# Kernel tuning notes

Measured on AMD Instinct MI355X. Metric: run time of the kernel, lower is better.

The kernel has to match this reference:

```python
import jax, jax.numpy as jnp
import numpy as np
from jax import lax

# Problem constants (match input_specs / init_kwargs)
B, N, F_IN = 16, 4096, 64          # clouds, points per cloud, feature dim
RATIO, R, K = 0.25, 0.1, 64        # fps ratio, ball radius, max neighbors
S = int(N * RATIO)                 # sampled centers per cloud (1024)
H1, H2, OUT = 64, 64, 128          # MLP [F_IN+3 -> 64 -> 64 -> 128]


def _fps(pos):
    """Farthest point sampling on one cloud. pos: [N,3] -> idx [S] (start at 0)."""
    def step(carry, _):
        mind, last = carry
        d = jnp.sum((pos - pos[last]) ** 2, axis=-1)
        mind = jnp.minimum(mind, d)
        nxt = jnp.argmax(mind)
        return (mind, nxt), nxt
    init = (jnp.full((pos.shape[0],), jnp.inf, pos.dtype), jnp.array(0))
    _, rest = lax.scan(step, init, None, length=S - 1)
    return jnp.concatenate([jnp.zeros((1,), rest.dtype), rest])


def _mlp(h, W1, b1, W2, b2, W3, b3):
    h = jax.nn.relu(h @ W1 + b1)
    h = jax.nn.relu(h @ W2 + b2)
    return jax.nn.relu(h @ W3 + b3)


def setup_inputs() -> dict:
    key = jax.random.key(0)
    ks = jax.random.split(key, 8)
    x = jax.random.normal(ks[0], (B * N, F_IN), jnp.float32)
    pos = jax.random.uniform(ks[1], (B * N, 3), jnp.float32)  # unit cube
    batch = jnp.arange(B * N, dtype=jnp.int64) // N           # cloud ids, equal-size clouds
    d_in = F_IN + 3
    W1 = jax.random.normal(ks[2], (d_in, H1), jnp.float32) / np.sqrt(d_in)
    b1 = jnp.zeros((H1,), jnp.float32)
    W2 = jax.random.normal(ks[3], (H1, H2), jnp.float32) / np.sqrt(H1)
    b2 = jnp.zeros((H2,), jnp.float32)
    W3 = jax.random.normal(ks[4], (H2, OUT), jnp.float32) / np.sqrt(H2)
    b3 = jnp.zeros((OUT,), jnp.float32)
    return {"x": x, "pos": pos, "batch": batch,
            "W1": W1, "b1": b1, "W2": W2, "b2": b2, "W3": W3, "b3": b3}


def reference(x, pos, batch, W1, b1, W2, b2, W3, b3):
    xb = x.reshape(B, N, F_IN)
    pb = pos.reshape(B, N, 3)
    # --- fps(pos, batch, ratio) : per-cloud farthest point sampling ---
    idx = jax.vmap(_fps)(pb)                                   # [B,S]
    pos_s = jnp.take_along_axis(pb, idx[:, :, None], axis=1)   # [B,S,3]
    # --- radius(pos, pos[idx], r, max_num_neighbors=K) : ball query ---
    d2 = jnp.sum((pos_s[:, :, None, :] - pb[:, None, :, :]) ** 2, axis=-1)  # [B,S,N]
    neg = jnp.where(d2 <= R * R, -d2, -jnp.inf)
    vals, nbr = lax.top_k(neg, K)                              # [B,S,K] nearest-in-ball
    valid = jnp.isfinite(vals)                                 # center is its own neighbor -> >=1 valid
    # --- PointNetConv: msg = nn(concat(x_j, pos_j - pos_i)), max aggregation ---
    x_j = jax.vmap(lambda a, i: a[i])(xb, nbr)                 # [B,S,K,F_IN]
    p_j = jax.vmap(lambda a, i: a[i])(pb, nbr)                 # [B,S,K,3]
    msg = jnp.concatenate([x_j, p_j - pos_s[:, :, None, :]], axis=-1)
    m = _mlp(msg, W1, b1, W2, b2, W3, b3)                      # [B,S,K,OUT]
    m = jnp.where(valid[..., None], m, -jnp.inf)
    out = jnp.max(m, axis=2)                                   # [B,S,OUT]
    batch_s = jnp.take_along_axis(batch.reshape(B, N), idx, axis=1).reshape(-1)
    return out.reshape(B * S, OUT), pos_s.reshape(B * S, 3), batch_s
```

## Files before the change

### kernel.cpp

```cpp
#include <hip/hip_runtime.h>
#include <hip/hip_bf16.h>
#include <math.h>


#define NB 16
#define NP 4096
#define FIN 64
#define NS 1024
#define KN 64
#define CAP 128
#define NCONS 240
#define NCHUNK 4096

typedef __attribute__((ext_vector_type(8))) short bf16x8;
typedef __attribute__((ext_vector_type(4))) float f32x4;

__device__ __forceinline__ float dist2e(float ax, float ay, float az,
                                        float bx, float by, float bz) {
    float dx = __fsub_rn(ax, bx);
    float dy = __fsub_rn(ay, by);
    float dz = __fsub_rn(az, bz);
    return __fadd_rn(__fadd_rn(__fmul_rn(dx, dx), __fmul_rn(dy, dy)),
                     __fmul_rn(dz, dz));
}

__device__ __forceinline__ short f2bf(float f) {
    unsigned u = __float_as_uint(f);
    unsigned r = (u + 0x7FFFu + ((u >> 16) & 1u)) >> 16;
    return (short)r;
}

#define DPP_KEY_MAX(k, CTRL)                                                   \
    do {                                                                       \
        int _lo = (int)(unsigned)((k) & 0xFFFFFFFFull);                        \
        int _hi = (int)(unsigned)((k) >> 32);                                  \
        int _plo = __builtin_amdgcn_update_dpp(_lo, _lo, CTRL, 0xF, 0xF, false);\
        int _phi = __builtin_amdgcn_update_dpp(_hi, _hi, CTRL, 0xF, 0xF, false);\
        unsigned long long _nk =                                               \
            ((unsigned long long)(unsigned)_phi << 32) | (unsigned)_plo;       \
        if (_nk > (k)) (k) = _nk;                                              \
    } while (0)

#define WAVE_KEY_MAX(k)                                                        \
    do {                                                                       \
        DPP_KEY_MAX(k, 0x121);                                                 \
        DPP_KEY_MAX(k, 0x122);                                                 \
        DPP_KEY_MAX(k, 0x124);                                                 \
        DPP_KEY_MAX(k, 0x128);                                                 \
        {                                                                      \
            int _lo = (int)(unsigned)((k) & 0xFFFFFFFFull);                    \
            int _hi = (int)(unsigned)((k) >> 32);                              \
            int _plo = __builtin_amdgcn_ds_swizzle(_lo, 0x401F);               \
            int _phi = __builtin_amdgcn_ds_swizzle(_hi, 0x401F);               \
            unsigned long long _nk =                                           \
                ((unsigned long long)(unsigned)_phi << 32) | (unsigned)_plo;   \
            if (_nk > (k)) (k) = _nk;                                          \
        }                                                                      \
        {                                                                      \
            unsigned long long _nk = __shfl_xor((k), 32, 64);                  \
            if (_nk > (k)) (k) = _nk;                                          \
        }                                                                      \
    } while (0)

#define SMEM_BYTES 65792

__global__ __launch_bounds__(256, 1) void fused_kernel(
        const float* __restrict__ pos, const float* __restrict__ x,
        const float* __restrict__ W1, const float* __restrict__ b1,
        const float* __restrict__ W2, const float* __restrict__ b2,
        const float* __restrict__ W3, const float* __restrict__ b3,
        float* __restrict__ out_feat, float* __restrict__ out_pos,
        float* __restrict__ out_batch, float* __restrict__ histg,
        int* __restrict__ progress) {
    __shared__ __align__(16) char smem[SMEM_BYTES];
    const int tid = threadIdx.x;
    const int lane = tid & 63;
    const int wv = tid >> 6;

    if (blockIdx.x < NB) {
        const int b = blockIdx.x;
        float* px = (float*)smem;
        float* py = (float*)(smem + 16384);
        float* pz = (float*)(smem + 32768);
        float4* hist = (float4*)(smem + 49152);
        float (*bc)[4][8] = (float(*)[4][8])(smem + 65536);
        const float* p = pos + (size_t)b * NP * 3;
        float lx[16], ly[16], lz[16], md[16];
#pragma unroll
        for (int i = 0; i < 16; ++i) {
            int j = tid + (i << 8);
            float xx = p[j * 3 + 0];
            float yy = p[j * 3 + 1];
            float zz = p[j * 3 + 2];
            px[j] = xx; py[j] = yy; pz[j] = zz;
            lx[i] = xx; ly[i] = yy; lz[i] = zz;
            md[i] = INFINITY;
        }
        __syncthreads();
        const float c0x = px[0], c0y = py[0], c0z = pz[0];
        float cx = c0x, cy = c0y, cz = c0z;
        if (tid == 0) hist[0] = make_float4(0.f, c0x, c0y, c0z);
        for (int s = 1; s < NS; ++s) {
            float bv = -1.0f;
            int bi = 0;
#pragma unroll
            for (int i = 0; i < 16; ++i) {
                float d = dist2e(lx[i], ly[i], lz[i], cx, cy, cz);
                float m = md[i];
                m = d < m ? d : m;
                md[i] = m;
                bool take = (m > bv);
                bv = take ? m : bv;
                bi = take ? (tid + (i << 8)) : bi;
            }
            unsigned long long key =
                ((unsigned long long)__float_as_uint(bv) << 32) |
                (unsigned)(~(unsigned)bi);
            WAVE_KEY_MAX(key);
            const int buf = s & 1;
            if (lane == 0) {
                int wi = (int)(~(unsigned)(key & 0xFFFFFFFFull));
                bc[buf][wv][0] =
                    __uint_as_float((unsigned)(key & 0xFFFFFFFFull));
                bc[buf][wv][1] = __uint_as_float((unsigned)(key >> 32));
                bc[buf][wv][2] = px[wi];
                bc[buf][wv][3] = py[wi];
                bc[buf][wv][4] = pz[wi];
            }
            __syncthreads();
            if ((s & 63) == 0) {
                const int base = s - 64;
                if (tid < 192) {
                    int cc = tid / 3, comp = tid % 3;
                    float4 h = hist[base + cc];
                    float v = comp == 0 ? h.y : (comp == 1 ? h.z : h.w);
                    __hip_atomic_store(
                        (unsigned*)&histg[((size_t)(b * NS + base + cc)) * 3 + comp],
                        __float_as_uint(v), __ATOMIC_RELAXED,
                        __HIP_MEMORY_SCOPE_AGENT);
                }
                __syncthreads();
                if (tid == 0)
                    __hip_atomic_store(&progress[b << 5], s, __ATOMIC_RELEASE,
                                       __HIP_MEMORY_SCOPE_AGENT);
            }
            unsigned long long bk;
            float bx, by, bz;
            {
                float4 e = *(const float4*)&bc[buf][0][0];
                bk = ((unsigned long long)__float_as_uint(e.y) << 32) |
                     __float_as_uint(e.x);
                bx = e.z; by = e.w; bz = bc[buf][0][4];
            }
#pragma unroll
            for (int w = 1; w < 4; ++w) {
                float4 e = *(const float4*)&bc[buf][w][0];
                unsigned long long k2 =
                    ((unsigned long long)__float_as_uint(e.y) << 32) |
                    __float_as_uint(e.x);
                float z2 = bc[buf][w][4];
                bool take = (k2 > bk);
                bk = take ? k2 : bk;
                bx = take ? e.z : bx;
                by = take ? e.w : by;
                bz = take ? z2 : bz;
            }
            const int cur = (int)(~(unsigned)(bk & 0xFFFFFFFFull));
            cx = bx; cy = by; cz = bz;
            if (tid == 0)
                hist[s] = make_float4(__int_as_float(cur), bx, by, bz);
        }
        __syncthreads();
        if (tid < 192) {
            int cc = tid / 3, comp = tid % 3;
            float4 h = hist[960 + cc];
            float v = comp == 0 ? h.y : (comp == 1 ? h.z : h.w);
            __hip_atomic_store(
                (unsigned*)&histg[((size_t)(b * NS + 960 + cc)) * 3 + comp],
                __float_as_uint(v), __ATOMIC_RELAXED, __HIP_MEMORY_SCOPE_AGENT);
        }
        __syncthreads();
        if (tid == 0)
            __hip_atomic_store(&progress[b << 5], NS, __ATOMIC_RELEASE,
                               __HIP_MEMORY_SCOPE_AGENT);
        for (int s = tid; s < NS; s += 256) {
            float4 e = hist[s];
            out_pos[(size_t)(b * NS + s) * 3 + 0] = e.y;
            out_pos[(size_t)(b * NS + s) * 3 + 1] = e.z;
            out_pos[(size_t)(b * NS + s) * 3 + 2] = e.w;
            out_batch[b * NS + s] = (float)b;
        }
        return;
    }

    const int w = blockIdx.x - NB;
    short* h1s = (short*)smem;
    short* h2s = (short*)(smem + 8192);
    float* cd2 = (float*)(smem + 16384);
    int*   cix = (int*)(smem + 18432);
    float* dpxA = (float*)(smem + 20480);
    float* dpyA = (float*)(smem + 21504);
    float* dpzA = (float*)(smem + 22528);
    int*   jA   = (int*)(smem + 23552);
    float* omax = (float*)(smem + 24576);
    int*   keepW = (int*)(smem + 26624);
    const int lg = lane >> 4;
    const int lr = lane & 15;
    bf16x8 w1f[3][4], w2f[2][4], w3f[2][8];
#pragma unroll
    for (int kt = 0; kt < 3; ++kt)
#pragma unroll
        for (int ct = 0; ct < 4; ++ct) {
            bf16x8 f;
#pragma unroll
            for (int i = 0; i < 8; ++i) {
                int k = 32 * kt + 8 * lg + i;
                float v = (k < 67) ? W1[k * 64 + 16 * ct + lr] : 0.f;
                f[i] = f2bf(v);
            }
            w1f[kt][ct] = f;
        }
#pragma unroll
    for (int kt = 0; kt < 2; ++kt)
#pragma unroll
        for (int ct = 0; ct < 4; ++ct) {
            bf16x8 f;
#pragma unroll
            for (int i = 0; i < 8; ++i) {
                int k = 32 * kt + 8 * lg + i;
                f[i] = f2bf(W2[k * 64 + 16 * ct + lr]);
            }
            w2f[kt][ct] = f;
        }
#pragma unroll
    for (int kt = 0; kt < 2; ++kt)
#pragma unroll
        for (int ct = 0; ct < 8; ++ct) {
            bf16x8 f;
#pragma unroll
            for (int i = 0; i < 8; ++i) {
                int k = 32 * kt + 8 * lg + i;
                f[i] = f2bf(W3[k * 128 + 16 * ct + lr]);
            }
            w3f[kt][ct] = f;
        }
    float b1v[4], b2v[4], b3v[8];
#pragma unroll
    for (int ct = 0; ct < 4; ++ct) {
        b1v[ct] = b1[16 * ct + lr];
        b2v[ct] = b2[16 * ct + lr];
    }
#pragma unroll
    for (int ct = 0; ct < 8; ++ct) b3v[ct] = b3[16 * ct + lr];

    for (int c = w; c < NCHUNK; c += NCONS) {
        const int s = c >> 2;
        const int bq = (c & 3) << 2;
        const int bw = bq + wv;
        while (__hip_atomic_load(&progress[bw << 5], __ATOMIC_ACQUIRE,
                                 __HIP_MEMORY_SCOPE_AGENT) <= s) {
            __builtin_amdgcn_s_sleep(16);
        }
        const size_t ho = ((size_t)(bw * NS + s)) * 3;
        const float ccx = __uint_as_float(__hip_atomic_load(
            (const unsigned*)&histg[ho + 0], __ATOMIC_RELAXED,
            __HIP_MEMORY_SCOPE_AGENT));
        const float ccy = __uint_as_float(__hip_atomic_load(
            (const unsigned*)&histg[ho + 1], __ATOMIC_RELAXED,
            __HIP_MEMORY_SCOPE_AGENT));
        const float ccz = __uint_as_float(__hip_atomic_load(
            (const unsigned*)&histg[ho + 2], __ATOMIC_RELAXED,
            __HIP_MEMORY_SCOPE_AGENT));
        int cnt = 0;
        const float* pcloud = pos + (size_t)bw * NP * 3;
        for (int it = 0; it < 64; ++it) {
            const int j = it * 64 + lane;
            const float* pp = pcloud + (size_t)j * 3;
            float d2 = dist2e(ccx, ccy, ccz, pp[0], pp[1], pp[2]);
            bool in = (d2 <= 0.01f);
            unsigned long long m = __ballot(in);
            if (in) {
                int slot = cnt + __popcll(m & ((1ull << lane) - 1ull));
                if (slot < CAP) {
                    cd2[wv * CAP + slot] = d2;
                    cix[wv * CAP + slot] = j;
                }
            }
            cnt += __popcll(m);
        }
        if (cnt > CAP) cnt = CAP;
        const int keep = cnt <= KN ? cnt : KN;
        if (lane == 0) keepW[wv] = keep;
        jA[wv * 64 + lane] = 0;
        if (cnt <= KN) {
            if (lane < keep) jA[wv * 64 + lane] = cix[wv * CAP + lane];
        } else {
            for (int e = lane; e < cnt; e += 64) {
                float d = cd2[wv * CAP + e];
                int id = cix[wv * CAP + e];
                int rank = 0;
                for (int q = 0; q < cnt; ++q) {
                    float dq = cd2[wv * CAP + q];
                    int iq = cix[wv * CAP + q];
                    rank += (dq < d || (dq == d && iq < id)) ? 1 : 0;
                }
                if (rank < KN) jA[wv * 64 + rank] = id;
            }
        }
        {
            int j = jA[wv * 64 + lane];
            const float* pp = pcloud + (size_t)j * 3;
            bool valid = lane < keep;
            dpxA[wv * 64 + lane] = valid ? (pp[0] - ccx) : 0.f;
            dpyA[wv * 64 + lane] = valid ? (pp[1] - ccy) : 0.f;
            dpzA[wv * 64 + lane] = valid ? (pp[2] - ccz) : 0.f;
        }
        __syncthreads();
        for (int cc = 0; cc < 4; ++cc) {
            const int C = keepW[cc];
            const int cen = (bq + cc) * NS + s;
            const int arow = 16 * wv + lr;
            bf16x8 a0, a1, a2;
            {
                const int jrow = (bq + cc) * NP + jA[cc * 64 + arow];
                const float* xr = x + (size_t)jrow * FIN + 8 * lg;
                float4 v0 = *(const float4*)(xr + 0);
                float4 v1 = *(const float4*)(xr + 4);
                float4 v2 = *(const float4*)(xr + 32);
                float4 v3 = *(const float4*)(xr + 36);
                a0[0] = f2bf(v0.x); a0[1] = f2bf(v0.y); a0[2] = f2bf(v0.z); a0[3] = f2bf(v0.w);
                a0[4] = f2bf(v1.x); a0[5] = f2bf(v1.y); a0[6] = f2bf(v1.z); a0[7] = f2bf(v1.w);
                a1[0] = f2bf(v2.x); a1[1] = f2bf(v2.y); a1[2] = f2bf(v2.z); a1[3] = f2bf(v2.w);
                a1[4] = f2bf(v3.x); a1[5] = f2bf(v3.y); a1[6] = f2bf(v3.z); a1[7] = f2bf(v3.w);
                float d0 = (lg == 0) ? dpxA[cc * 64 + arow] : 0.f;
                float d1 = (lg == 0) ? dpyA[cc * 64 + arow] : 0.f;
                float d2v = (lg == 0) ? dpzA[cc * 64 + arow] : 0.f;
                a2[0] = f2bf(d0); a2[1] = f2bf(d1); a2[2] = f2bf(d2v);
                a2[3] = 0; a2[4] = 0; a2[5] = 0; a2[6] = 0; a2[7] = 0;
            }
            {
                f32x4 acc[4];
#pragma unroll
                for (int ct = 0; ct < 4; ++ct) {
                    acc[ct] = (f32x4){b1v[ct], b1v[ct], b1v[ct], b1v[ct]};
                    acc[ct] = __builtin_amdgcn_mfma_f32_16x16x32_bf16(a0, w1f[0][ct], acc[ct], 0, 0, 0);
                    acc[ct] = __builtin_amdgcn_mfma_f32_16x16x32_bf16(a1, w1f[1][ct], acc[ct], 0, 0, 0);
                    acc[ct] = __builtin_amdgcn_mfma_f32_16x16x32_bf16(a2, w1f[2][ct], acc[ct], 0, 0, 0);
                }
#pragma unroll
                for (int ct = 0; ct < 4; ++ct)
#pragma unroll
                    for (int r = 0; r < 4; ++r) {
                        int rw = 16 * wv + 4 * lg + r;
                        int idx = rw * 64 + 16 * ct + lr;
                        h1s[idx ^ ((rw & 7) << 3)] = f2bf(fmaxf(acc[ct][r], 0.f));
                    }
            }
            bf16x8 ha0 = *(bf16x8*)&h1s[(arow * 64 + 0  + 8 * lg) ^ ((arow & 7) << 3)];
            bf16x8 ha1 = *(bf16x8*)&h1s[(arow * 64 + 32 + 8 * lg) ^ ((arow & 7) << 3)];
            {
                f32x4 acc[4];
#pragma unroll
                for (int ct = 0; ct < 4; ++ct) {
                    acc[ct] = (f32x4){b2v[ct], b2v[ct], b2v[ct], b2v[ct]};
                    acc[ct] = __builtin_amdgcn_mfma_f32_16x16x32_bf16(ha0, w2f[0][ct], acc[ct], 0, 0, 0);
                    acc[ct] = __builtin_amdgcn_mfma_f32_16x16x32_bf16(ha1, w2f[1][ct], acc[ct], 0, 0, 0);
                }
#pragma unroll
                for (int ct = 0; ct < 4; ++ct)
#pragma unroll
                    for (int r = 0; r < 4; ++r) {
                        int rw = 16 * wv + 4 * lg + r;
                        int idx = rw * 64 + 16 * ct + lr;
                        h2s[idx ^ ((rw & 7) << 3)] = f2bf(fmaxf(acc[ct][r], 0.f));
                    }
            }
            bf16x8 hb0 = *(bf16x8*)&h2s[(arow * 64 + 0  + 8 * lg) ^ ((arow & 7) << 3)];
            bf16x8 hb1 = *(bf16x8*)&h2s[(arow * 64 + 32 + 8 * lg) ^ ((arow & 7) << 3)];
            {
                f32x4 acc3[8];
#pragma unroll
                for (int ct = 0; ct < 8; ++ct) {
                    acc3[ct] = (f32x4){b3v[ct], b3v[ct], b3v[ct], b3v[ct]};
                    acc3[ct] = __builtin_amdgcn_mfma_f32_16x16x32_bf16(hb0, w3f[0][ct], acc3[ct], 0, 0, 0);
                    acc3[ct] = __builtin_amdgcn_mfma_f32_16x16x32_bf16(hb1, w3f[1][ct], acc3[ct], 0, 0, 0);
                }
#pragma unroll
                for (int ct = 0; ct < 8; ++ct) {
                    float m = -INFINITY;
#pragma unroll
                    for (int r = 0; r < 4; ++r) {
                        int rg = 16 * wv + 4 * lg + r;
                        float v = fmaxf(acc3[ct][r], 0.f);
                        m = (rg < C && v > m) ? v : m;
                    }
                    m = fmaxf(m, __shfl_xor(m, 16, 64));
                    m = fmaxf(m, __shfl_xor(m, 32, 64));
                    if (lg == 0) omax[wv * 128 + 16 * ct + lr] = m;
                }
            }
            __syncthreads();
            if (tid < 128) {
                float m = fmaxf(fmaxf(omax[0 * 128 + tid], omax[1 * 128 + tid]),
                                fmaxf(omax[2 * 128 + tid], omax[3 * 128 + tid]));
                out_feat[(size_t)cen * 128 + tid] = m;
            }
            __syncthreads();
        }
    }
}

extern "C" void kernel_launch(void* const* d_in, const int* in_sizes, int n_in,
                              void* d_out, int out_size, void* d_ws, size_t ws_size,
                              hipStream_t stream) {
    const float* x   = (const float*)d_in[0];
    const float* pos = (const float*)d_in[1];
    const float* W1  = (const float*)d_in[3];
    const float* b1  = (const float*)d_in[4];
    const float* W2  = (const float*)d_in[5];
    const float* b2  = (const float*)d_in[6];
    const float* W3  = (const float*)d_in[7];
    const float* b3  = (const float*)d_in[8];
    float* out = (float*)d_out;
    char* ws = (char*)d_ws;
    int*   progress = (int*)ws;
    float* histg    = (float*)(ws + 4096);
    float* out_feat  = out;
    float* out_pos   = out + (size_t)16384 * 128;
    float* out_batch = out + (size_t)16384 * 131;
    hipMemsetAsync(ws, 0, 4096, stream);
    fused_kernel<<<256, 256, 0, stream>>>(pos, x, W1, b1, W2, b2, W3, b3,
                                          out_feat, out_pos, out_batch,
                                          histg, progress);
}
```

Baseline: 1.009 ms.

## Run FPS on a single wave with packed math, offload publishing to a second wave

```diff
diff --git a/kernel.cpp b/kernel.cpp
--- a/kernel.cpp
+++ b/kernel.cpp
@@ -14,6 +14,7 @@
 
 typedef __attribute__((ext_vector_type(8))) short bf16x8;
 typedef __attribute__((ext_vector_type(4))) float f32x4;
+typedef __attribute__((ext_vector_type(2))) float f32x2;
 
 __device__ __forceinline__ float dist2e(float ax, float ay, float az,
                                         float bx, float by, float bz) {
@@ -62,7 +63,7 @@
         }                                                                      \
     } while (0)
 
-#define SMEM_BYTES 65792
+#define SMEM_BYTES 65600
 
 __global__ __launch_bounds__(256, 1) void fused_kernel(
         const float* __restrict__ pos, const float* __restrict__ x,
@@ -80,115 +81,125 @@
     if (blockIdx.x < NB) {
         const int b = blockIdx.x;
         float* px = (float*)smem;
-        float* py = (float*)(smem + 16384);
-        float* pz = (float*)(smem + 32768);
+        float* py = px + NP;
+        float* pz = py + NP;
         float4* hist = (float4*)(smem + 49152);
-        float (*bc)[4][8] = (float(*)[4][8])(smem + 65536);
+        int* cnt = (int*)(smem + 65536);
         const float* p = pos + (size_t)b * NP * 3;
-        float lx[16], ly[16], lz[16], md[16];
-#pragma unroll
         for (int i = 0; i < 16; ++i) {
             int j = tid + (i << 8);
-            float xx = p[j * 3 + 0];
-            float yy = p[j * 3 + 1];
-            float zz = p[j * 3 + 2];
-            px[j] = xx; py[j] = yy; pz[j] = zz;
-            lx[i] = xx; ly[i] = yy; lz[i] = zz;
-            md[i] = INFINITY;
+            px[j] = p[j * 3 + 0];
+            py[j] = p[j * 3 + 1];
+            pz[j] = p[j * 3 + 2];
+        }
+        if (tid == 0) {
+            *cnt = 0;
+            hist[0] = make_float4(0.f, p[0], p[1], p[2]);
         }
         __syncthreads();
-        const float c0x = px[0], c0y = py[0], c0z = pz[0];
-        float cx = c0x, cy = c0y, cz = c0z;
-        if (tid == 0) hist[0] = make_float4(0.f, c0x, c0y, c0z);
-        for (int s = 1; s < NS; ++s) {
-            float bv = -1.0f;
-            int bi = 0;
-#pragma unroll
-            for (int i = 0; i < 16; ++i) {
-                float d = dist2e(lx[i], ly[i], lz[i], cx, cy, cz);
-                float m = md[i];
-                m = d < m ? d : m;
-                md[i] = m;
-                bool take = (m > bv);
-                bv = take ? m : bv;
-                bi = take ? (tid + (i << 8)) : bi;
-            }
-            unsigned long long key =
-                ((unsigned long long)__float_as_uint(bv) << 32) |
-                (unsigned)(~(unsigned)bi);
-            WAVE_KEY_MAX(key);
-            const int buf = s & 1;
-            if (lane == 0) {
-                int wi = (int)(~(unsigned)(key & 0xFFFFFFFFull));
-                bc[buf][wv][0] =
-                    __uint_as_float((unsigned)(key & 0xFFFFFFFFull));
-                bc[buf][wv][1] = __uint_as_float((unsigned)(key >> 32));
-                bc[buf][wv][2] = px[wi];
-                bc[buf][wv][3] = py[wi];
-                bc[buf][wv][4] = pz[wi];
-            }
-            __syncthreads();
-            if ((s & 63) == 0) {
-                const int base = s - 64;
-                if (tid < 192) {
-                    int cc = tid / 3, comp = tid % 3;
-                    float4 h = hist[base + cc];
-                    float v = comp == 0 ? h.y : (comp == 1 ? h.z : h.w);
-                    __hip_atomic_store(
-                        (unsigned*)&histg[((size_t)(b * NS + base + cc)) * 3 + comp],
-                        __float_as_uint(v), __ATOMIC_RELAXED,
-                        __HIP_MEMORY_SCOPE_AGENT);
-                }
-                __syncthreads();
-                if (tid == 0)
-                    __hip_atomic_store(&progress[b << 5], s, __ATOMIC_RELEASE,
+
+        if (wv == 0) {
+            f32x2 lx2[32], ly2[32], lz2[32], md2[32];
+#pragma unroll
+            for (int k = 0; k < 32; ++k) {
+#pragma unroll
+                for (int e = 0; e < 2; ++e) {
+                    int j = ((2 * k + e) << 6) | lane;
+                    lx2[k][e] = px[j];
+                    ly2[k][e] = py[j];
+                    lz2[k][e] = pz[j];
+                }
+                md2[k] = (f32x2){INFINITY, INFINITY};
+            }
+            float cx = px[0], cy = py[0], cz = pz[0];
+            for (int s = 1; s < NS; ++s) {
+                {
+#pragma clang fp contract(off)
+                    const f32x2 cx2 = (f32x2){cx, cx};
+                    const f32x2 cy2 = (f32x2){cy, cy};
+                    const f32x2 cz2 = (f32x2){cz, cz};
+#pragma unroll
+                    for (int k = 0; k < 32; ++k) {
+                        f32x2 dx = lx2[k] - cx2;
+                        f32x2 dy = ly2[k] - cy2;
+                        f32x2 dz = lz2[k] - cz2;
+                        f32x2 d = (dx * dx + dy * dy) + dz * dz;
+                        f32x2 m = md2[k];
+                        m[0] = d[0] < m[0] ? d[0] : m[0];
+                        m[1] = d[1] < m[1] ? d[1] : m[1];
+                        md2[k] = m;
+                    }
+                }
+                float v0 = -1.f, v1 = -1.f, v2 = -1.f, v3 = -1.f;
+                int e0 = 0, e1 = 0, e2 = 0, e3 = 0;
+#pragma unroll
+                for (int m4 = 0; m4 < 16; ++m4) {
+                    float a0 = md2[2 * m4][0];
+                    float a1 = md2[2 * m4][1];
+                    float a2 = md2[2 * m4 + 1][0];
+                    float a3 = md2[2 * m4 + 1][1];
+                    bool t;
+                    t = a0 > v0; v0 = t ? a0 : v0; e0 = t ? (4 * m4 + 0) : e0;
+                    t = a1 > v1; v1 = t ? a1 : v1; e1 = t ? (4 * m4 + 1) : e1;
+                    t = a2 > v2; v2 = t ? a2 : v2; e2 = t ? (4 * m4 + 2) : e2;
+                    t = a3 > v3; v3 = t ? a3 : v3; e3 = t ? (4 * m4 + 3) : e3;
+                }
+                bool t01 = (v1 > v0) || (v1 == v0 && e1 < e0);
+                float va = t01 ? v1 : v0;
+                int ea = t01 ? e1 : e0;
+                bool t23 = (v3 > v2) || (v3 == v2 && e3 < e2);
+                float vb = t23 ? v3 : v2;
+                int eb = t23 ? e3 : e2;
+                bool tab = (vb > va) || (vb == va && eb < ea);
+                float bv = tab ? vb : va;
+                int bi = ((tab ? eb : ea) << 6) | lane;
+                unsigned long long key =
+                    ((unsigned long long)__float_as_uint(bv) << 32) |
+                    (unsigned)(~(unsigned)bi);
+                WAVE_KEY_MAX(key);
+                const int wi = (int)(~(unsigned)(key & 0xFFFFFFFFull));
+                cx = px[wi];
+                cy = py[wi];
+                cz = pz[wi];
+                if (lane == 0) {
+                    hist[s] = make_float4(__int_as_float(wi), cx, cy, cz);
+                    __hip_atomic_store(cnt, s, __ATOMIC_RELEASE,
+                                       __HIP_MEMORY_SCOPE_WORKGROUP);
+                }
+            }
+            return;
+        }
+        if (wv == 1) {
+            for (int chunk = 0; chunk < 16; ++chunk) {
+                const int base = chunk * 64;
+                const int need = base + 63;
+                while (__hip_atomic_load(cnt, __ATOMIC_ACQUIRE,
+                                         __HIP_MEMORY_SCOPE_WORKGROUP) < need) {
+                    __builtin_amdgcn_s_sleep(32);
+                }
+                const int e = base + lane;
+                float4 h = hist[e];
+                const int gi = b * NS + e;
+                __hip_atomic_store((unsigned*)&histg[(size_t)gi * 3 + 0],
+                                   __float_as_uint(h.y), __ATOMIC_RELAXED,
+                                   __HIP_MEMORY_SCOPE_AGENT);
+                __hip_atomic_store((unsigned*)&histg[(size_t)gi * 3 + 1],
+                                   __float_as_uint(h.z), __ATOMIC_RELAXED,
+                                   __HIP_MEMORY_SCOPE_AGENT);
+                __hip_atomic_store((unsigned*)&histg[(size_t)gi * 3 + 2],
+                                   __float_as_uint(h.w), __ATOMIC_RELAXED,
+                                   __HIP_MEMORY_SCOPE_AGENT);
+                out_pos[(size_t)gi * 3 + 0] = h.y;
+                out_pos[(size_t)gi * 3 + 1] = h.z;
+                out_pos[(size_t)gi * 3 + 2] = h.w;
+                out_batch[gi] = (float)b;
+                asm volatile("s_waitcnt vmcnt(0)" ::: "memory");
+                if (lane == 0)
+                    __hip_atomic_store(&progress[b << 5], base + 64,
+                                       __ATOMIC_RELEASE,
                                        __HIP_MEMORY_SCOPE_AGENT);
             }
-            unsigned long long bk;
-            float bx, by, bz;
-            {
-                float4 e = *(const float4*)&bc[buf][0][0];
-                bk = ((unsigned long long)__float_as_uint(e.y) << 32) |
-                     __float_as_uint(e.x);
-                bx = e.z; by = e.w; bz = bc[buf][0][4];
-            }
-#pragma unroll
-            for (int w = 1; w < 4; ++w) {
-                float4 e = *(const float4*)&bc[buf][w][0];
-                unsigned long long k2 =
-                    ((unsigned long long)__float_as_uint(e.y) << 32) |
-                    __float_as_uint(e.x);
-                float z2 = bc[buf][w][4];
-                bool take = (k2 > bk);
-                bk = take ? k2 : bk;
-                bx = take ? e.z : bx;
-                by = take ? e.w : by;
-                bz = take ? z2 : bz;
-            }
-            const int cur = (int)(~(unsigned)(bk & 0xFFFFFFFFull));
-            cx = bx; cy = by; cz = bz;
-            if (tid == 0)
-                hist[s] = make_float4(__int_as_float(cur), bx, by, bz);
-        }
-        __syncthreads();
-        if (tid < 192) {
-            int cc = tid / 3, comp = tid % 3;
-            float4 h = hist[960 + cc];
-            float v = comp == 0 ? h.y : (comp == 1 ? h.z : h.w);
-            __hip_atomic_store(
-                (unsigned*)&histg[((size_t)(b * NS + 960 + cc)) * 3 + comp],
-                __float_as_uint(v), __ATOMIC_RELAXED, __HIP_MEMORY_SCOPE_AGENT);
-        }
-        __syncthreads();
-        if (tid == 0)
-            __hip_atomic_store(&progress[b << 5], NS, __ATOMIC_RELEASE,
-                               __HIP_MEMORY_SCOPE_AGENT);
-        for (int s = tid; s < NS; s += 256) {
-            float4 e = hist[s];
-            out_pos[(size_t)(b * NS + s) * 3 + 0] = e.y;
-            out_pos[(size_t)(b * NS + s) * 3 + 1] = e.z;
-            out_pos[(size_t)(b * NS + s) * 3 + 2] = e.w;
-            out_batch[b * NS + s] = (float)b;
+            return;
         }
         return;
     }
@@ -271,7 +282,7 @@
         const float ccz = __uint_as_float(__hip_atomic_load(
             (const unsigned*)&histg[ho + 2], __ATOMIC_RELAXED,
             __HIP_MEMORY_SCOPE_AGENT));
-        int cnt = 0;
+        int cnt2 = 0;
         const float* pcloud = pos + (size_t)bw * NP * 3;
         for (int it = 0; it < 64; ++it) {
             const int j = it * 64 + lane;
@@ -280,26 +291,26 @@
             bool in = (d2 <= 0.01f);
             unsigned long long m = __ballot(in);
             if (in) {
-                int slot = cnt + __popcll(m & ((1ull << lane) - 1ull));
+                int slot = cnt2 + __popcll(m & ((1ull << lane) - 1ull));
                 if (slot < CAP) {
                     cd2[wv * CAP + slot] = d2;
                     cix[wv * CAP + slot] = j;
                 }
             }
-            cnt += __popcll(m);
-        }
-        if (cnt > CAP) cnt = CAP;
-        const int keep = cnt <= KN ? cnt : KN;
+            cnt2 += __popcll(m);
+        }
+        if (cnt2 > CAP) cnt2 = CAP;
+        const int keep = cnt2 <= KN ? cnt2 : KN;
         if (lane == 0) keepW[wv] = keep;
         jA[wv * 64 + lane] = 0;
-        if (cnt <= KN) {
+        if (cnt2 <= KN) {
             if (lane < keep) jA[wv * 64 + lane] = cix[wv * CAP + lane];
         } else {
-            for (int e = lane; e < cnt; e += 64) {
+            for (int e = lane; e < cnt2; e += 64) {
                 float d = cd2[wv * CAP + e];
                 int id = cix[wv * CAP + e];
                 int rank = 0;
-                for (int q = 0; q < cnt; ++q) {
+                for (int q = 0; q < cnt2; ++q) {
                     float dq = cd2[wv * CAP + q];
                     int iq = cix[wv * CAP + q];
                     rank += (dq < d || (dq == d && iq < id)) ? 1 : 0;
```

New measurement: 1.824 ms. 80.8% more time.
